# Performance work log

Measured on AMD Instinct MI355X. Metric: run time of the kernel, lower is better.

## Reference

```python
import jax, jax.numpy as jnp
import numpy as np

D_MODEL = 1024
NUM_HEADS = 16
D_K = D_MODEL // NUM_HEADS
LN_EPS = 1e-5


def setup_inputs() -> dict:
    key = jax.random.key(0)
    ks = jax.random.split(key, 16)
    B, SQ, SK = 2, 2048, 2048
    s = 1.0 / np.sqrt(D_MODEL)
    inp = {
        "query": jax.random.normal(ks[0], (B, SQ, D_MODEL), jnp.float32),
        "key": jax.random.normal(ks[1], (B, SK, D_MODEL), jnp.float32),
        "value": jax.random.normal(ks[2], (B, SK, D_MODEL), jnp.float32),
        "mask": jax.random.randint(ks[3], (B, SQ, SK), 0, 2, jnp.int32),
        "w_q": jax.random.normal(ks[4], (D_MODEL, D_MODEL), jnp.float32) * s,
        "b_q": jnp.zeros((D_MODEL,), jnp.float32),
        "w_k": jax.random.normal(ks[5], (D_MODEL, D_MODEL), jnp.float32) * s,
        "b_k": jnp.zeros((D_MODEL,), jnp.float32),
        "w_v": jax.random.normal(ks[6], (D_MODEL, D_MODEL), jnp.float32) * s,
        "b_v": jnp.zeros((D_MODEL,), jnp.float32),
        "w_o": jax.random.normal(ks[7], (D_MODEL, D_MODEL), jnp.float32) * s,
        "b_o": jnp.zeros((D_MODEL,), jnp.float32),
        "ln_gamma": jnp.ones((D_MODEL,), jnp.float32),
        "ln_beta": jnp.zeros((D_MODEL,), jnp.float32),
    }
    return inp


def _split_heads(x):
    B, S, _ = x.shape
    return x.reshape(B, S, NUM_HEADS, D_K).transpose(0, 2, 1, 3)  # [B,H,S,Dk]


def reference(query, key, value, mask, w_q, b_q, w_k, b_k, w_v, b_v, w_o, b_o, ln_gamma, ln_beta):
    residual = query
    # torch Linear: y = x @ W.T + b
    Q = _split_heads(jnp.einsum('bsd,ed->bse', query, w_q) + b_q)
    K = _split_heads(jnp.einsum('bsd,ed->bse', key, w_k) + b_k)
    V = _split_heads(jnp.einsum('bsd,ed->bse', value, w_v) + b_v)
    scores = jnp.einsum('bhqd,bhkd->bhqk', Q, K) / jnp.sqrt(jnp.float32(D_K))
    scores = jnp.where(mask[:, None, :, :] == 0, jnp.float32(-1e9), scores)
    attn = jax.nn.softmax(scores, axis=-1)
    # dropout: eval mode (identity)
    ctx = jnp.einsum('bhqk,bhkd->bhqd', attn, V)
    B, H, SQ, Dk = ctx.shape
    ctx = ctx.transpose(0, 2, 1, 3).reshape(B, SQ, D_MODEL)
    out = jnp.einsum('bsd,ed->bse', ctx, w_o) + b_o + residual
    mu = jnp.mean(out, axis=-1, keepdims=True)
    var = jnp.mean(jnp.square(out - mu), axis=-1, keepdims=True)
    out = (out - mu) * jax.lax.rsqrt(var + LN_EPS) * ln_gamma + ln_beta
    return out
```

## Files before the change

### kernel.cpp

```cpp
#include <hip/hip_runtime.h>

typedef unsigned short u16;
typedef __attribute__((ext_vector_type(8))) short bf16x8;
typedef __attribute__((ext_vector_type(4))) float f32x4;

#define LOG2E 1.4426950408889634f
#define QSCALE (LOG2E / 8.0f)

__device__ __forceinline__ u16 f2bf(float f) {
  union { float f; unsigned u; } v; v.f = f;
  unsigned r = v.u + 0x7fffu + ((v.u >> 16) & 1u);
  return (u16)(r >> 16);
}

__device__ __forceinline__ void gload_lds16(const void* g, void* l) {
  __builtin_amdgcn_global_load_lds(
      (const __attribute__((address_space(1))) unsigned int*)(unsigned long long)g,
      (__attribute__((address_space(3))) unsigned int*)(unsigned int)(unsigned long long)l,
      16, 0, 0);
}

__global__ __launch_bounds__(256) void prep_kernel(
    const float* __restrict__ q, const float* __restrict__ k, const float* __restrict__ v,
    const float* __restrict__ wq, const float* __restrict__ wk, const float* __restrict__ wv,
    const float* __restrict__ wo, const int* __restrict__ mask,
    u16* __restrict__ Xq, u16* __restrict__ Xk, u16* __restrict__ Xv,
    u16* __restrict__ Wq, u16* __restrict__ Wk, u16* __restrict__ Wv, u16* __restrict__ Wo,
    unsigned long long* __restrict__ Mp) {
  const int bx = blockIdx.x;
  if (bx < 16384) {
    const float* src; u16* dst; float sc; int idx;
    if (bx < 12288) {
      int seg = bx >> 12;
      idx = (bx & 4095) * 256 + threadIdx.x;
      src = seg == 0 ? q : (seg == 1 ? k : v);
      dst = seg == 0 ? Xq : (seg == 1 ? Xk : Xv);
      sc = 1.f;
    } else {
      int t = bx - 12288, seg = t >> 10;
      idx = (t & 1023) * 256 + threadIdx.x;
      src = seg == 0 ? wq : (seg == 1 ? wk : (seg == 2 ? wv : wo));
      dst = seg == 0 ? Wq : (seg == 1 ? Wk : (seg == 2 ? Wv : Wo));
      sc = seg == 0 ? QSCALE : 1.f;
    }
    float4 x = ((const float4*)src)[idx];
    ushort4 o;
    o.x = f2bf(x.x * sc); o.y = f2bf(x.y * sc);
    o.z = f2bf(x.z * sc); o.w = f2bf(x.w * sc);
    ((ushort4*)dst)[idx] = o;
  } else {
    int gw = (((bx - 16384) * 256) + threadIdx.x) >> 6;
    int lane = threadIdx.x & 63;
    for (int w = gw; w < 131072; w += 16384) {
      int m = mask[(size_t)w * 64 + lane];
      unsigned long long b = __ballot(m != 0);
      if (lane == 0) Mp[w] = b;
    }
  }
}

__global__ __launch_bounds__(256, 3) void gemm_kernel(
    const u16* __restrict__ Xq, const u16* __restrict__ Xk, const u16* __restrict__ Xv,
    const u16* __restrict__ Wq, const u16* __restrict__ Wk, const u16* __restrict__ Wv,
    const u16* __restrict__ Wo, const u16* __restrict__ Ctx,
    const float* __restrict__ bq, const float* __restrict__ bk, const float* __restrict__ bv,
    u16* __restrict__ Qd, u16* __restrict__ Kd, u16* __restrict__ Vtd, float* __restrict__ outp,
    int mode_base) {
  __shared__ __align__(16) u16 SH[17408];
  u16* As = SH;
  u16* Bs = SH + 4096;
  const int mode = mode_base + blockIdx.z;
  const int tid = threadIdx.x;
  const int wid = tid >> 6, l = tid & 63, quad = l >> 4, ln = l & 15;
  const int wm = wid >> 1, wn = wid & 1;

  const u16 *A, *B; const float* bias;
  if (mode == 0)      { A = Wq; B = Xq;  bias = bq; }
  else if (mode == 1) { A = Wk; B = Xk;  bias = bk; }
  else if (mode == 2) { A = Xv; B = Wv;  bias = bv; }
  else                { A = Wo; B = Ctx; bias = bq; }
  int mBase, nBase;
  if (mode == 2) { mBase = blockIdx.x * 128; nBase = blockIdx.y * 128; }
  else           { mBase = blockIdx.y * 128; nBase = blockIdx.x * 128; }

  const u16* Ag = A + (size_t)mBase * 1024;
  const u16* Bg = B + (size_t)nBase * 1024;

  f32x4 acc[4][4] = {};

  for (int k0 = 0; k0 < 1024; k0 += 32) {
    if (k0) __syncthreads();
    {
      int i0 = tid, i1 = tid + 256;
      gload_lds16(Ag + (size_t)(i0 & 127) * 1024 + k0 + (i0 >> 7) * 8, &As[i0 * 8]);
      gload_lds16(Ag + (size_t)(i1 & 127) * 1024 + k0 + (i1 >> 7) * 8, &As[i1 * 8]);
      gload_lds16(Bg + (size_t)(i0 & 127) * 1024 + k0 + (i0 >> 7) * 8, &Bs[i0 * 8]);
      gload_lds16(Bg + (size_t)(i1 & 127) * 1024 + k0 + (i1 >> 7) * 8, &Bs[i1 * 8]);
    }
    __syncthreads();
    bf16x8 af[4], bf[4];
#pragma unroll
    for (int i = 0; i < 4; ++i)
      af[i] = *(const bf16x8*)&As[(quad * 128 + wm * 64 + i * 16 + ln) * 8];
#pragma unroll
    for (int j = 0; j < 4; ++j)
      bf[j] = *(const bf16x8*)&Bs[(quad * 128 + wn * 64 + j * 16 + ln) * 8];
#pragma unroll
    for (int i = 0; i < 4; ++i)
#pragma unroll
      for (int j = 0; j < 4; ++j)
        acc[i][j] = __builtin_amdgcn_mfma_f32_16x16x32_bf16(af[i], bf[j], acc[i][j], 0, 0, 0);
  }

  __syncthreads();

  if (mode <= 1) {
    const float bscale = (mode == 0) ? QSCALE : 1.0f;
#pragma unroll
    for (int i = 0; i < 4; ++i) {
      int f0 = wm * 64 + i * 16 + quad * 4;
      float4 bb = *(const float4*)(bias + mBase + f0);
#pragma unroll
      for (int j = 0; j < 4; ++j) {
        int sl = wn * 64 + j * 16 + ln;
        f32x4 v = acc[i][j];
        ushort4 o;
        o.x = f2bf(v[0] + bb.x * bscale); o.y = f2bf(v[1] + bb.y * bscale);
        o.z = f2bf(v[2] + bb.z * bscale); o.w = f2bf(v[3] + bb.w * bscale);
        *(ushort4*)&SH[sl * 136 + f0] = o;
      }
    }
    __syncthreads();
    u16* dstQK = (mode == 0) ? Qd : Kd;
#pragma unroll
    for (int p = 0; p < 8; ++p) {
      int sl = p * 16 + (tid >> 4);
      int fl = (tid & 15) * 8;
      uint4 w = *(const uint4*)&SH[sl * 136 + fl];
      int s = nBase + sl, f = mBase + fl;
      int h = f >> 6, d = f & 63, b = s >> 11, sr = s & 2047;
      *(uint4*)(dstQK + (((size_t)(b * 16 + h) * 2048 + sr) * 64 + d)) = w;
    }
  } else if (mode == 2) {
#pragma unroll
    for (int j = 0; j < 4; ++j) {
      int fl = wn * 64 + j * 16 + ln;
      float bb = bias[nBase + fl];
#pragma unroll
      for (int i = 0; i < 4; ++i) {
        int s0 = wm * 64 + i * 16 + quad * 4;
        f32x4 v = acc[i][j];
        ushort4 o;
        o.x = f2bf(v[0] + bb); o.y = f2bf(v[1] + bb);
        o.z = f2bf(v[2] + bb); o.w = f2bf(v[3] + bb);
        *(ushort4*)&SH[fl * 136 + s0] = o;
      }
    }
    __syncthreads();
#pragma unroll
    for (int p = 0; p < 8; ++p) {
      int fl = p * 16 + (tid >> 4);
      int sl = (tid & 15) * 8;
      uint4 w = *(const uint4*)&SH[fl * 136 + sl];
      int f = nBase + fl, s = mBase + sl;
      int h = f >> 6, d = f & 63, b = s >> 11, sr = s & 2047;
      *(uint4*)(Vtd + (((size_t)(b * 16 + h) * 64 + d) * 2048 + sr)) = w;
    }
  } else {
    float* ES = (float*)SH;
#pragma unroll
    for (int h2 = 0; h2 < 2; ++h2) {
      if (h2) __syncthreads();
      if (wn == h2) {
#pragma unroll
        for (int i = 0; i < 4; ++i) {
          int f0 = wm * 64 + i * 16 + quad * 4;
#pragma unroll
          for (int j = 0; j < 4; ++j) {
            int sl = j * 16 + ln;
            f32x4 v = acc[i][j];
            float4 o; o.x = v[0]; o.y = v[1]; o.z = v[2]; o.w = v[3];
            *(float4*)&ES[sl * 132 + f0] = o;
          }
        }
      }
      __syncthreads();
#pragma unroll
      for (int p = 0; p < 8; ++p) {
        int sl = p * 8 + (tid >> 5);
        int fl = (tid & 31) * 4;
        float4 w = *(const float4*)&ES[sl * 132 + fl];
        int s = nBase + h2 * 64 + sl;
        *(float4*)(outp + (size_t)s * 1024 + mBase + fl) = w;
      }
    }
  }
}

__global__ __launch_bounds__(256, 2) void attn_kernel(
    const u16* __restrict__ Qg, const u16* __restrict__ Kg, const u16* __restrict__ Vtg,
    const unsigned* __restrict__ Mp, u16* __restrict__ ctx) {
  __shared__ __align__(16) u16 Ks0[8192];
  __shared__ __align__(16) u16 Ks1[8192];
  __shared__ __align__(16) u16 Vs0[8192];
  __shared__ __align__(16) u16 Vs1[8192];
  __shared__ __align__(16) u16 Ps[8192];
  const int tid = threadIdx.x;
  const int wid = tid >> 6, l = tid & 63, quad = l >> 4, ln = l & 15;
  const int q4 = quad * 4;
  const int L = blockIdx.x;
  const int bh = (L & 7) + 8 * (L >> 7);
  const int b = bh >> 4, h = bh & 15;
  const int qBase = ((L >> 3) & 15) * 128;
  const int wq = wid * 32;
  const int sw = (ln & 7) << 3;

  bf16x8 qf[2][2];
#pragma unroll
  for (int qt = 0; qt < 2; ++qt)
#pragma unroll
    for (int kc = 0; kc < 2; ++kc)
      qf[qt][kc] = *(const bf16x8*)(Qg + (((size_t)bh * 2048 + qBase + wq + qt * 16 + ln) * 64 +
                                          kc * 32 + quad * 8));

  f32x4 oacc[2][4] = {};
  f32x4 lsum[2] = {};
  const bf16x8 vone = {(short)0x3F80, (short)0x3F80, (short)0x3F80, (short)0x3F80,
                       (short)0x3F80, (short)0x3F80, (short)0x3F80, (short)0x3F80};

  const unsigned* mrow[2];
  mrow[0] = Mp + ((size_t)b * 2048 + qBase + wq + ln) * 64;
  mrow[1] = mrow[0] + 16 * 64;

  const u16* KgB = Kg + (size_t)bh * 2048 * 64;
  const u16* VgB = Vtg + (size_t)bh * 64 * 2048;

#define STAGE_TILE(KS, VS, t_)                                                  \
  do {                                                                          \
    const int kvB_ = (t_) * 128;                                                \
    _Pragma("unroll")                                                           \
    for (int r_ = 0; r_ < 4; ++r_) {                                            \
      int c_ = r_ * 256 + tid;                                                  \
      gload_lds16(KgB + (size_t)(kvB_ + (c_ & 127)) * 64 + (c_ >> 7) * 8,       \
                  &KS[c_ * 8]);                                                 \
      gload_lds16(VgB + (size_t)(c_ & 63) * 2048 + kvB_ + (c_ >> 6) * 8,        \
                  &VS[c_ * 8]);                                                 \
    }                                                                           \
  } while (0)

#define COMPUTE_TILE(KS, VS, it_)                                                         \
  do {                                                                                    \
    unsigned ww[2][4];                                                                    \
    {                                                                                     \
      uint4 m0 = *(const uint4*)(mrow[0] + (it_) * 4);                                    \
      uint4 m1 = *(const uint4*)(mrow[1] + (it_) * 4);                                    \
      ww[0][0] = m0.x; ww[0][1] = m0.y; ww[0][2] = m0.z; ww[0][3] = m0.w;                 \
      ww[1][0] = m1.x; ww[1][1] = m1.y; ww[1][2] = m1.z; ww[1][3] = m1.w;                 \
    }                                                                                     \
    _Pragma("unroll")                                                                     \
    for (int hf = 0; hf < 2; ++hf) {                                                      \
      f32x4 s[4][2];                                                                      \
      _Pragma("unroll")                                                                   \
      for (int m2 = 0; m2 < 4; ++m2) {                                                    \
        int mt = hf * 4 + m2;                                                             \
        bf16x8 k0 = *(const bf16x8*)&KS[((0 + quad) * 128 + mt * 16 + ln) * 8];           \
        bf16x8 k1 = *(const bf16x8*)&KS[((4 + quad) * 128 + mt * 16 + ln) * 8];           \
        _Pragma("unroll")                                                                 \
        for (int qt = 0; qt < 2; ++qt) {                                                  \
          f32x4 z = {0.f, 0.f, 0.f, 0.f};                                                 \
          z = __builtin_amdgcn_mfma_f32_16x16x32_bf16(k0, qf[qt][0], z, 0, 0, 0);         \
          s[m2][qt] = __builtin_amdgcn_mfma_f32_16x16x32_bf16(k1, qf[qt][1], z, 0, 0, 0); \
        }                                                                                 \
      }                                                                                   \
      uint2 pk[4][2];                                                                     \
      _Pragma("unroll")                                                                   \
      for (int qt = 0; qt < 2; ++qt)                                                      \
        _Pragma("unroll")                                                                 \
        for (int m2 = 0; m2 < 4; ++m2) {                                                  \
          int mt = hf * 4 + m2;                                                           \
          unsigned nib = (ww[qt][mt >> 1] >> ((mt & 1) * 16 + q4)) & 0xFu;                \
          float p0 = __builtin_amdgcn_exp2f((nib & 1u) ? s[m2][qt][0] : -1e30f);          \
          float p1 = __builtin_amdgcn_exp2f((nib & 2u) ? s[m2][qt][1] : -1e30f);          \
          float p2 = __builtin_amdgcn_exp2f((nib & 4u) ? s[m2][qt][2] : -1e30f);          \
          float p3 = __builtin_amdgcn_exp2f((nib & 8u) ? s[m2][qt][3] : -1e30f);          \
          pk[m2][qt].x = __builtin_amdgcn_perm(__float_as_uint(p1) + 0x8000u,             \
                                               __float_as_uint(p0) + 0x8000u, 0x07060302u); \
          pk[m2][qt].y = __builtin_amdgcn_perm(__float_as_uint(p3) + 0x8000u,             \
                                               __float_as_uint(p2) + 0x8000u, 0x07060302u); \
        }                                                                                 \
              \
      _Pragma("unroll")                                                                   \
      for (int qt = 0; qt < 2; ++qt) {                                                    \
        int qrow = wq + qt * 16 + ln;                                                     \
        _Pragma("unroll")                                                                 \
        for (int m2 = 0; m2 < 4; ++m2)                                                    \
          *(uint2*)&Ps[(qrow * 64 + m2 * 16 + q4) ^ sw] = pk[m2][qt];                     \
      }                                                                                   \
      _Pragma("unroll")                                                                   \
      for (int k2 = 0; k2 < 2; ++k2) {                                                    \
        int kc2 = hf * 2 + k2;                                                            \
        bf16x8 aP[2];                                                                     \
        _Pragma("unroll")                                                                 \
        for (int qt = 0; qt < 2; ++qt)                                                    \
          aP[qt] = *(const bf16x8*)&Ps[((wq + qt * 16 + ln) * 64 + k2 * 32 + quad * 8) ^ sw]; \
        _Pragma("unroll")                                                                 \
        for (int nt = 0; nt < 4; ++nt) {                                                  \
          bf16x8 bV = *(const bf16x8*)&VS[((kc2 * 4 + quad) * 64 + nt * 16 + ln) * 8];    \
          _Pragma("unroll")                                                               \
          for (int qt = 0; qt < 2; ++qt)                                                  \
            oacc[qt][nt] = __builtin_amdgcn_mfma_f32_16x16x32_bf16(aP[qt], bV, oacc[qt][nt], 0, 0, 0); \
        }                                                                                 \
        _Pragma("unroll")                                                                 \
        for (int qt = 0; qt < 2; ++qt)                                                    \
          lsum[qt] = __builtin_amdgcn_mfma_f32_16x16x32_bf16(aP[qt], vone, lsum[qt], 0, 0, 0); \
      }                                                                                   \
    }                                                                                     \
  } while (0)

  STAGE_TILE(Ks0, Vs0, 0);
#pragma unroll 1
  for (int it2 = 0; it2 < 8; ++it2) {
    __syncthreads();
    STAGE_TILE(Ks1, Vs1, 2 * it2 + 1);
    COMPUTE_TILE(Ks0, Vs0, 2 * it2);
    __syncthreads();
    if (it2 < 7) STAGE_TILE(Ks0, Vs0, 2 * it2 + 2);
    COMPUTE_TILE(Ks1, Vs1, 2 * it2 + 1);
  }
#undef STAGE_TILE
#undef COMPUTE_TILE

  __syncthreads();
#pragma unroll
  for (int qt = 0; qt < 2; ++qt)
#pragma unroll
    for (int r = 0; r < 4; ++r) {
      float il = 1.0f / lsum[qt][r];
      int q = wq + qt * 16 + q4 + r;
#pragma unroll
      for (int nt = 0; nt < 4; ++nt)
        Ps[q * 64 + nt * 16 + ln] = f2bf(oacc[qt][nt][r] * il);
    }
  __syncthreads();
#pragma unroll
  for (int r = 0; r < 4; ++r) {
    int c = r * 256 + tid;
    int q = c >> 3, ch = c & 7;
    *(uint4*)(ctx + ((size_t)(b * 2048 + qBase + q) * 1024 + h * 64 + ch * 8)) =
        *(const uint4*)&Ps[q * 64 + ch * 8];
  }
}

__global__ __launch_bounds__(256) void ln_kernel(const float* __restrict__ x,
                                                 const float* __restrict__ resid,
                                                 const float* __restrict__ bo,
                                                 const float* __restrict__ gamma,
                                                 const float* __restrict__ beta,
                                                 float* __restrict__ out) {
  __shared__ float red[8];
  const int tid = threadIdx.x;
  const size_t row = blockIdx.x;
  float4 v = ((const float4*)(x + row * 1024))[tid];
  const float4 rr = ((const float4*)(resid + row * 1024))[tid];
  const float4 bb = ((const float4*)bo)[tid];
  v.x += rr.x + bb.x; v.y += rr.y + bb.y; v.z += rr.z + bb.z; v.w += rr.w + bb.w;
  float s1 = v.x + v.y + v.z + v.w;
  float s2 = v.x * v.x + v.y * v.y + v.z * v.z + v.w * v.w;
#pragma unroll
  for (int o = 32; o >= 1; o >>= 1) {
    s1 += __shfl_xor(s1, o);
    s2 += __shfl_xor(s2, o);
  }
  if ((tid & 63) == 0) { red[(tid >> 6) * 2] = s1; red[(tid >> 6) * 2 + 1] = s2; }
  __syncthreads();
  s1 = red[0] + red[2] + red[4] + red[6];
  s2 = red[1] + red[3] + red[5] + red[7];
  float mu = s1 * (1.f / 1024.f);
  float var = s2 * (1.f / 1024.f) - mu * mu;
  float inv = rsqrtf(var + 1e-5f);
  float4 g = ((const float4*)gamma)[tid];
  float4 be = ((const float4*)beta)[tid];
  float4 o;
  o.x = (v.x - mu) * inv * g.x + be.x;
  o.y = (v.y - mu) * inv * g.y + be.y;
  o.z = (v.z - mu) * inv * g.z + be.z;
  o.w = (v.w - mu) * inv * g.w + be.w;
  ((float4*)(out + row * 1024))[tid] = o;
}

extern "C" void kernel_launch(void* const* d_in, const int* in_sizes, int n_in,
                              void* d_out, int out_size, void* d_ws, size_t ws_size,
                              hipStream_t stream) {
  const float* query = (const float*)d_in[0];
  const float* key   = (const float*)d_in[1];
  const float* value = (const float*)d_in[2];
  const int*   mask  = (const int*)d_in[3];
  const float* w_q = (const float*)d_in[4];
  const float* b_q = (const float*)d_in[5];
  const float* w_k = (const float*)d_in[6];
  const float* b_k = (const float*)d_in[7];
  const float* w_v = (const float*)d_in[8];
  const float* b_v = (const float*)d_in[9];
  const float* w_o = (const float*)d_in[10];
  const float* b_o = (const float*)d_in[11];
  const float* ln_g = (const float*)d_in[12];
  const float* ln_b = (const float*)d_in[13];
  float* out = (float*)d_out;

  char* ws = (char*)d_ws;
  u16* Xq = (u16*)(ws + ((size_t)0 << 20));
  u16* Xk = (u16*)(ws + ((size_t)8 << 20));
  u16* Xv = (u16*)(ws + ((size_t)16 << 20));
  float* outpre = (float*)(ws + ((size_t)8 << 20));
  u16* Wq = (u16*)(ws + ((size_t)24 << 20));
  u16* Wk = (u16*)(ws + ((size_t)26 << 20));
  u16* Wv = (u16*)(ws + ((size_t)28 << 20));
  u16* Wo = (u16*)(ws + ((size_t)30 << 20));
  u16* Qd = (u16*)(ws + ((size_t)32 << 20));
  u16* Kd = (u16*)(ws + ((size_t)40 << 20));
  u16* Vtd = (u16*)(ws + ((size_t)48 << 20));
  unsigned long long* Mp = (unsigned long long*)(ws + ((size_t)56 << 20));
  u16* ctx = Xq;

  prep_kernel<<<20480, 256, 0, stream>>>(query, key, value, w_q, w_k, w_v, w_o, mask,
                                         Xq, Xk, Xv, Wq, Wk, Wv, Wo, Mp);
  gemm_kernel<<<dim3(32, 8, 3), 256, 0, stream>>>(Xq, Xk, Xv, Wq, Wk, Wv, Wo, ctx,
      b_q, b_k, b_v, Qd, Kd, Vtd, outpre, 0);
  attn_kernel<<<dim3(512), 256, 0, stream>>>(Qd, Kd, Vtd, (const unsigned*)Mp, ctx);
  gemm_kernel<<<dim3(32, 8, 1), 256, 0, stream>>>(Xq, Xk, Xv, Wq, Wk, Wv, Wo, ctx,
      b_q, b_k, b_v, Qd, Kd, Vtd, outpre, 3);
  ln_kernel<<<4096, 256, 0, stream>>>(outpre, query, b_o, ln_g, ln_b, out);
}
```

Measured before the change: 316.6 us.

## Halve attention tiles to 64x64, double grid, raise occupancy with setprio

Cuts the attention block from 128 query rows per block (32 per wave) to 64 (16 per wave) and the KV tile from 128 to 64 keys. LDS and register use drop, so launch bounds allow 4 blocks per CU and the grid doubles to 1024 blocks. s_setprio is placed around the MFMA phases to help interleave work across waves. It also drops the +0x8000 rounding in the bf16 pack of P, so values are truncated. The cost is half the K/V reuse per loaded tile, twice as many barriers and loop iterations, and slightly lower precision.

```diff
diff --git a/kernel.cpp b/kernel.cpp
--- a/kernel.cpp
+++ b/kernel.cpp
@@ -197,51 +197,47 @@
   }
 }
 
-__global__ __launch_bounds__(256, 2) void attn_kernel(
+__global__ __launch_bounds__(256, 4) void attn_kernel(
     const u16* __restrict__ Qg, const u16* __restrict__ Kg, const u16* __restrict__ Vtg,
     const unsigned* __restrict__ Mp, u16* __restrict__ ctx) {
-  __shared__ __align__(16) u16 Ks0[8192];
-  __shared__ __align__(16) u16 Ks1[8192];
-  __shared__ __align__(16) u16 Vs0[8192];
-  __shared__ __align__(16) u16 Vs1[8192];
-  __shared__ __align__(16) u16 Ps[8192];
+  __shared__ __align__(16) u16 Ks0[4096];
+  __shared__ __align__(16) u16 Ks1[4096];
+  __shared__ __align__(16) u16 Vs0[4096];
+  __shared__ __align__(16) u16 Vs1[4096];
+  __shared__ __align__(16) u16 Ps[4096];
   const int tid = threadIdx.x;
   const int wid = tid >> 6, l = tid & 63, quad = l >> 4, ln = l & 15;
   const int q4 = quad * 4;
   const int L = blockIdx.x;
-  const int bh = (L & 7) + 8 * (L >> 7);
+  const int bh = (L & 7) + 8 * (L >> 8);
   const int b = bh >> 4, h = bh & 15;
-  const int qBase = ((L >> 3) & 15) * 128;
-  const int wq = wid * 32;
+  const int qBase = ((L >> 3) & 31) * 64;
+  const int wq = wid * 16;
   const int sw = (ln & 7) << 3;
 
-  bf16x8 qf[2][2];
-#pragma unroll
-  for (int qt = 0; qt < 2; ++qt)
-#pragma unroll
-    for (int kc = 0; kc < 2; ++kc)
-      qf[qt][kc] = *(const bf16x8*)(Qg + (((size_t)bh * 2048 + qBase + wq + qt * 16 + ln) * 64 +
-                                          kc * 32 + quad * 8));
-
-  f32x4 oacc[2][4] = {};
-  f32x4 lsum[2] = {};
+  bf16x8 qf[2];
+#pragma unroll
+  for (int kc = 0; kc < 2; ++kc)
+    qf[kc] = *(const bf16x8*)(Qg + (((size_t)bh * 2048 + qBase + wq + ln) * 64 +
+                                    kc * 32 + quad * 8));
+
+  f32x4 oacc[4] = {};
+  f32x4 lsum = {};
   const bf16x8 vone = {(short)0x3F80, (short)0x3F80, (short)0x3F80, (short)0x3F80,
                        (short)0x3F80, (short)0x3F80, (short)0x3F80, (short)0x3F80};
 
-  const unsigned* mrow[2];
-  mrow[0] = Mp + ((size_t)b * 2048 + qBase + wq + ln) * 64;
-  mrow[1] = mrow[0] + 16 * 64;
+  const unsigned* mrow = Mp + ((size_t)b * 2048 + qBase + wq + ln) * 64;
 
   const u16* KgB = Kg + (size_t)bh * 2048 * 64;
   const u16* VgB = Vtg + (size_t)bh * 64 * 2048;
 
 #define STAGE_TILE(KS, VS, t_)                                                  \
   do {                                                                          \
-    const int kvB_ = (t_) * 128;                                                \
+    const int kvB_ = (t_) * 64;                                                 \
     _Pragma("unroll")                                                           \
-    for (int r_ = 0; r_ < 4; ++r_) {                                            \
+    for (int r_ = 0; r_ < 2; ++r_) {                                            \
       int c_ = r_ * 256 + tid;                                                  \
-      gload_lds16(KgB + (size_t)(kvB_ + (c_ & 127)) * 64 + (c_ >> 7) * 8,       \
+      gload_lds16(KgB + (size_t)(kvB_ + (c_ & 63)) * 64 + (c_ >> 6) * 8,        \
                   &KS[c_ * 8]);                                                 \
       gload_lds16(VgB + (size_t)(c_ & 63) * 2048 + kvB_ + (c_ >> 6) * 8,        \
                   &VS[c_ * 8]);                                                 \
@@ -250,81 +246,61 @@
 
 #define COMPUTE_TILE(KS, VS, it_)                                                         \
   do {                                                                                    \
-    unsigned ww[2][4];                                                                    \
+    unsigned ww[2];                                                                       \
     {                                                                                     \
-      uint4 m0 = *(const uint4*)(mrow[0] + (it_) * 4);                                    \
-      uint4 m1 = *(const uint4*)(mrow[1] + (it_) * 4);                                    \
-      ww[0][0] = m0.x; ww[0][1] = m0.y; ww[0][2] = m0.z; ww[0][3] = m0.w;                 \
-      ww[1][0] = m1.x; ww[1][1] = m1.y; ww[1][2] = m1.z; ww[1][3] = m1.w;                 \
+      uint2 m0 = *(const uint2*)(mrow + (it_) * 2);                                       \
+      ww[0] = m0.x; ww[1] = m0.y;                                                         \
     }                                                                                     \
+    f32x4 s[4];                                                                           \
+    __builtin_amdgcn_s_setprio(1);                                                        \
     _Pragma("unroll")                                                                     \
-    for (int hf = 0; hf < 2; ++hf) {                                                      \
-      f32x4 s[4][2];                                                                      \
+    for (int m2 = 0; m2 < 4; ++m2) {                                                      \
+      bf16x8 k0 = *(const bf16x8*)&KS[((0 + quad) * 64 + m2 * 16 + ln) * 8];              \
+      bf16x8 k1 = *(const bf16x8*)&KS[((4 + quad) * 64 + m2 * 16 + ln) * 8];              \
+      f32x4 z = {0.f, 0.f, 0.f, 0.f};                                                     \
+      z = __builtin_amdgcn_mfma_f32_16x16x32_bf16(k0, qf[0], z, 0, 0, 0);                 \
+      s[m2] = __builtin_amdgcn_mfma_f32_16x16x32_bf16(k1, qf[1], z, 0, 0, 0);             \
+    }                                                                                     \
+    __builtin_amdgcn_s_setprio(0);                                                        \
+    uint2 pk[4];                                                                          \
+    _Pragma("unroll")                                                                     \
+    for (int m2 = 0; m2 < 4; ++m2) {                                                      \
+      unsigned nib = (ww[m2 >> 1] >> ((m2 & 1) * 16 + q4)) & 0xFu;                        \
+      float p0 = __builtin_amdgcn_exp2f((nib & 1u) ? s[m2][0] : -1e30f);                  \
+      float p1 = __builtin_amdgcn_exp2f((nib & 2u) ? s[m2][1] : -1e30f);                  \
+      float p2 = __builtin_amdgcn_exp2f((nib & 4u) ? s[m2][2] : -1e30f);                  \
+      float p3 = __builtin_amdgcn_exp2f((nib & 8u) ? s[m2][3] : -1e30f);                  \
+      pk[m2].x = __builtin_amdgcn_perm(__float_as_uint(p1), __float_as_uint(p0),          \
+                                       0x07060302u);                                      \
+      pk[m2].y = __builtin_amdgcn_perm(__float_as_uint(p3), __float_as_uint(p2),          \
+                                       0x07060302u);                                      \
+    }                                                                                     \
+              \
+    _Pragma("unroll")                                                                     \
+    for (int m2 = 0; m2 < 4; ++m2)                                                        \
+      *(uint2*)&Ps[(((wq + ln) * 64) + m2 * 16 + q4) ^ sw] = pk[m2];                      \
+    __builtin_amdgcn_s_setprio(1);                                                        \
+    _Pragma("unroll")                                                                     \
+    for (int k2 = 0; k2 < 2; ++k2) {                                                      \
+      bf16x8 aP = *(const bf16x8*)&Ps[(((wq + ln) * 64) + k2 * 32 + quad * 8) ^ sw];      \
       _Pragma("unroll")                                                                   \
-      for (int m2 = 0; m2 < 4; ++m2) {                                                    \
-        int mt = hf * 4 + m2;                                                             \
-        bf16x8 k0 = *(const bf16x8*)&KS[((0 + quad) * 128 + mt * 16 + ln) * 8];           \
-        bf16x8 k1 = *(const bf16x8*)&KS[((4 + quad) * 128 + mt * 16 + ln) * 8];           \
-        _Pragma("unroll")                                                                 \
-        for (int qt = 0; qt < 2; ++qt) {                                                  \
-          f32x4 z = {0.f, 0.f, 0.f, 0.f};                                                 \
-          z = __builtin_amdgcn_mfma_f32_16x16x32_bf16(k0, qf[qt][0], z, 0, 0, 0);         \
-          s[m2][qt] = __builtin_amdgcn_mfma_f32_16x16x32_bf16(k1, qf[qt][1], z, 0, 0, 0); \
-        }                                                                                 \
+      for (int nt = 0; nt < 4; ++nt) {                                                    \
+        bf16x8 bV = *(const bf16x8*)&VS[((k2 * 4 + quad) * 64 + nt * 16 + ln) * 8];       \
+        oacc[nt] = __builtin_amdgcn_mfma_f32_16x16x32_bf16(aP, bV, oacc[nt], 0, 0, 0);    \
       }                                                                                   \
-      uint2 pk[4][2];                                                                     \
-      _Pragma("unroll")                                                                   \
-      for (int qt = 0; qt < 2; ++qt)                                                      \
-        _Pragma("unroll")                                                                 \
-        for (int m2 = 0; m2 < 4; ++m2) {                                                  \
-          int mt = hf * 4 + m2;                                                           \
-          unsigned nib = (ww[qt][mt >> 1] >> ((mt & 1) * 16 + q4)) & 0xFu;                \
-          float p0 = __builtin_amdgcn_exp2f((nib & 1u) ? s[m2][qt][0] : -1e30f);          \
-          float p1 = __builtin_amdgcn_exp2f((nib & 2u) ? s[m2][qt][1] : -1e30f);          \
-          float p2 = __builtin_amdgcn_exp2f((nib & 4u) ? s[m2][qt][2] : -1e30f);          \
-          float p3 = __builtin_amdgcn_exp2f((nib & 8u) ? s[m2][qt][3] : -1e30f);          \
-          pk[m2][qt].x = __builtin_amdgcn_perm(__float_as_uint(p1) + 0x8000u,             \
-                                               __float_as_uint(p0) + 0x8000u, 0x07060302u); \
-          pk[m2][qt].y = __builtin_amdgcn_perm(__float_as_uint(p3) + 0x8000u,             \
-                                               __float_as_uint(p2) + 0x8000u, 0x07060302u); \
-        }                                                                                 \
-              \
-      _Pragma("unroll")                                                                   \
-      for (int qt = 0; qt < 2; ++qt) {                                                    \
-        int qrow = wq + qt * 16 + ln;                                                     \
-        _Pragma("unroll")                                                                 \
-        for (int m2 = 0; m2 < 4; ++m2)                                                    \
-          *(uint2*)&Ps[(qrow * 64 + m2 * 16 + q4) ^ sw] = pk[m2][qt];                     \
-      }                                                                                   \
-      _Pragma("unroll")                                                                   \
-      for (int k2 = 0; k2 < 2; ++k2) {                                                    \
-        int kc2 = hf * 2 + k2;                                                            \
-        bf16x8 aP[2];                                                                     \
-        _Pragma("unroll")                                                                 \
-        for (int qt = 0; qt < 2; ++qt)                                                    \
-          aP[qt] = *(const bf16x8*)&Ps[((wq + qt * 16 + ln) * 64 + k2 * 32 + quad * 8) ^ sw]; \
-        _Pragma("unroll")                                                                 \
-        for (int nt = 0; nt < 4; ++nt) {                                                  \
-          bf16x8 bV = *(const bf16x8*)&VS[((kc2 * 4 + quad) * 64 + nt * 16 + ln) * 8];    \
-          _Pragma("unroll")                                                               \
-          for (int qt = 0; qt < 2; ++qt)                                                  \
-            oacc[qt][nt] = __builtin_amdgcn_mfma_f32_16x16x32_bf16(aP[qt], bV, oacc[qt][nt], 0, 0, 0); \
-        }                                                                                 \
-        _Pragma("unroll")                                                                 \
-        for (int qt = 0; qt < 2; ++qt)                                                    \
-          lsum[qt] = __builtin_amdgcn_mfma_f32_16x16x32_bf16(aP[qt], vone, lsum[qt], 0, 0, 0); \
-      }                                                                                   \
+      lsum = __builtin_amdgcn_mfma_f32_16x16x32_bf16(aP, vone, lsum, 0, 0, 0);            \
     }                                                                                     \
+    __builtin_amdgcn_s_setprio(0);                                                        \
   } while (0)
 
   STAGE_TILE(Ks0, Vs0, 0);
 #pragma unroll 1
-  for (int it2 = 0; it2 < 8; ++it2) {
+  for (int it2 = 0; it2 < 16; ++it2) {
     __syncthreads();
     STAGE_TILE(Ks1, Vs1, 2 * it2 + 1);
     COMPUTE_TILE(Ks0, Vs0, 2 * it2);
     __syncthreads();
-    if (it2 < 7) STAGE_TILE(Ks0, Vs0, 2 * it2 + 2);
+    if (it2 < 15) STAGE_TILE(Ks0, Vs0, 2 * it2 + 2);
     COMPUTE_TILE(Ks1, Vs1, 2 * it2 + 1);
   }
 #undef STAGE_TILE
@@ -332,18 +308,16 @@
 
   __syncthreads();
 #pragma unroll
-  for (int qt = 0; qt < 2; ++qt)
-#pragma unroll
-    for (int r = 0; r < 4; ++r) {
-      float il = 1.0f / lsum[qt][r];
-      int q = wq + qt * 16 + q4 + r;
-#pragma unroll
-      for (int nt = 0; nt < 4; ++nt)
-        Ps[q * 64 + nt * 16 + ln] = f2bf(oacc[qt][nt][r] * il);
-    }
+  for (int r = 0; r < 4; ++r) {
+    float il = 1.0f / lsum[r];
+    int q = wq + q4 + r;
+#pragma unroll
+    for (int nt = 0; nt < 4; ++nt)
+      Ps[q * 64 + nt * 16 + ln] = f2bf(oacc[nt][r] * il);
+  }
   __syncthreads();
 #pragma unroll
-  for (int r = 0; r < 4; ++r) {
+  for (int r = 0; r < 2; ++r) {
     int c = r * 256 + tid;
     int q = c >> 3, ch = c & 7;
     *(uint4*)(ctx + ((size_t)(b * 2048 + qBase + q) * 1024 + h * 64 + ch * 8)) =
@@ -426,7 +400,7 @@
                                          Xq, Xk, Xv, Wq, Wk, Wv, Wo, Mp);
   gemm_kernel<<<dim3(32, 8, 3), 256, 0, stream>>>(Xq, Xk, Xv, Wq, Wk, Wv, Wo, ctx,
       b_q, b_k, b_v, Qd, Kd, Vtd, outpre, 0);
-  attn_kernel<<<dim3(512), 256, 0, stream>>>(Qd, Kd, Vtd, (const unsigned*)Mp, ctx);
+  attn_kernel<<<dim3(1024), 256, 0, stream>>>(Qd, Kd, Vtd, (const unsigned*)Mp, ctx);
   gemm_kernel<<<dim3(32, 8, 1), 256, 0, stream>>>(Xq, Xk, Xv, Wq, Wk, Wv, Wo, ctx,
       b_q, b_k, b_v, Qd, Kd, Vtd, outpre, 3);
   ln_kernel<<<4096, 256, 0, stream>>>(outpre, query, b_o, ln_g, ln_b, out);
```

Measured after the change: 329.7 us. 1.04x slower.
